# Kernel optimization log

Measured on AMD Instinct MI355X. Metric: run time of the kernel, lower is better.

## Reference

```python
import jax, jax.numpy as jnp
import numpy as np

NUM_GRAPHS = 4096
NODES_PER_GRAPH = 24
EDGES_PER_GRAPH = 48
LG_EDGES_PER_GRAPH = 144
N_ITER = 4
HID = 128
IN_DIM = 70
EDGE_DIM = 6


def seg_softmax(v, seg, num_seg):
    # numerically-stable softmax over segments; v: [E,1]
    m = jax.ops.segment_max(v, seg, num_segments=num_seg)
    e = jnp.exp(v - m[seg])
    s = jax.ops.segment_sum(e, seg, num_segments=num_seg)
    return e / s[seg]


def setup_inputs() -> dict:
    key = jax.random.key(0)
    ks = jax.random.split(key, 20)
    B, NPG, EPG, LPG = NUM_GRAPHS, NODES_PER_GRAPH, EDGES_PER_GRAPH, LG_EDGES_PER_GRAPH
    N, E, LE = B * NPG, B * EPG, B * LPG
    # graph-consistent random connectivity
    goff_n = (jnp.arange(B, dtype=jnp.int32) * NPG)[:, None]
    src = (goff_n + jax.random.randint(ks[0], (B, EPG), 0, NPG)).reshape(-1)
    dst = (goff_n + jax.random.randint(ks[1], (B, EPG), 0, NPG)).reshape(-1)
    edge_index = jnp.stack([src, dst]).astype(jnp.int32)
    goff_e = (jnp.arange(B, dtype=jnp.int32) * EPG)[:, None]
    lsrc = (goff_e + jax.random.randint(ks[2], (B, LPG), 0, EPG)).reshape(-1)
    ldst = (goff_e + jax.random.randint(ks[3], (B, LPG), 0, EPG)).reshape(-1)
    lg_edge_index = jnp.stack([lsrc, ldst]).astype(jnp.int32)
    edge_batch = jnp.repeat(jnp.arange(B, dtype=jnp.int32), EPG)
    s = 0.1
    inp = {
        "x": jax.random.normal(ks[4], (N, IN_DIM), jnp.float32),
        "edge_attr": jax.random.normal(ks[5], (E, EDGE_DIM), jnp.float32),
        "edge_index": edge_index,
        "lg_edge_index": lg_edge_index,
        "edge_batch": edge_batch,
        # params (stored [in, out] so we apply x @ W + b)
        "w_mlp": jax.random.normal(ks[6], (IN_DIM, HID), jnp.float32) * s,
        "b_mlp": jnp.zeros((HID,), jnp.float32),
        "w_u": jax.random.normal(ks[7], (HID, HID), jnp.float32) * s,
        "w_v": jax.random.normal(ks[8], (HID, HID), jnp.float32) * s,
        "w_edge": jax.random.normal(ks[9], (EDGE_DIM, HID), jnp.float32) * s,
        "w_rel": jax.random.normal(ks[10], (HID, 1), jnp.float32) * s,
        "b_rel": jnp.zeros((1,), jnp.float32),
        "w_root": jax.random.normal(ks[11], (HID, 1), jnp.float32) * s,
        "a": jax.random.normal(ks[12], (1, HID, N_ITER), jnp.float32) * s,
        "a_bias": jnp.zeros((1, 1, N_ITER), jnp.float32),
        "w_gout": jax.random.normal(ks[13], (HID, HID), jnp.float32) * s,
        "b_gout": jnp.zeros((HID,), jnp.float32),
        "w_block": jax.random.normal(ks[14], (HID, HID), jnp.float32) * s,
        "b_block": jnp.zeros((HID,), jnp.float32),
    }
    return inp


def reference(x, edge_attr, edge_index, lg_edge_index, edge_batch,
              w_mlp, b_mlp, w_u, w_v, w_edge, w_rel, b_rel, w_root,
              a, a_bias, w_gout, b_gout, w_block, b_block):
    N = x.shape[0]
    src, dst = edge_index[0], edge_index[1]
    lsrc, ldst = lg_edge_index[0], lg_edge_index[1]
    E = src.shape[0]

    # DrugEncoder.mlp
    h = x @ w_mlp + b_mlp  # [N, H]

    # initial directed-edge features: (lin_u(x)[src] + lin_v(x)[dst] + lin_edge(e)) / 3
    e0 = (h @ w_u)[src] + (h @ w_v)[dst] + edge_attr @ w_edge
    e0 = e0 / 3.0  # [E, H]

    out = e0
    outs, gouts = [], []
    for _ in range(N_ITER):
        # line-graph message passing: scatter-add over line-graph edges
        out = e0 + jax.ops.segment_sum(out[lsrc], ldst, num_segments=E)
        # GlobalAttentionPool: GraphConv(H->1) on the line graph, segment softmax, weighted add-pool
        aggr = jax.ops.segment_sum(out[lsrc], ldst, num_segments=E)
        xc = aggr @ w_rel + b_rel + out @ w_root  # [E, 1]
        sc = seg_softmax(xc, edge_batch, NUM_GRAPHS)  # [E, 1]
        g = jax.ops.segment_sum(out * sc, edge_batch, num_segments=NUM_GRAPHS)  # [B, H]
        outs.append(out)
        gouts.append(jnp.tanh(g @ w_gout + b_gout))

    out_all = jnp.stack(outs, axis=-1)    # [E, H, T]
    gout_all = jnp.stack(gouts, axis=-1)  # [B, H, T]

    # temporal attention over iterations
    scores = jnp.einsum('bht,ht->bt', gout_all, a[0])[:, None, :] + a_bias  # [B,1,T]
    scores = jax.nn.softmax(scores, axis=-1)
    per_edge = scores[edge_batch]  # gather == repeat_interleave by per-graph edge counts
    out = (out_all * per_edge).sum(-1)  # [E, H]

    # scatter edge features back to destination nodes
    xo = h + jax.ops.segment_sum(out, dst, num_segments=N)
    xo = xo @ w_block + b_block  # LinearBlock.lin1
    return xo
```

## Files before the change

### kernel.cpp

```cpp
#include <hip/hip_runtime.h>

#define NGR 4096
#define NPG 24
#define EPG 48
#define LPG 144
#define NITER 4
#define HID 128
#define NN (NGR*NPG)
#define NE (NGR*EPG)
#define NL (NGR*LPG)

typedef unsigned int uint;
typedef unsigned short ushort;
typedef short bf16x8 __attribute__((ext_vector_type(8)));
typedef float f32x4 __attribute__((ext_vector_type(4)));
typedef float f32x2 __attribute__((ext_vector_type(2)));

__device__ __forceinline__ float b2f(ushort u){ return __uint_as_float(((uint)u)<<16); }
__device__ __forceinline__ ushort f2b(float f){
  uint x = __float_as_uint(f);
  x += 0x7FFFu + ((x>>16)&1u);
  return (ushort)(x>>16);
}
__device__ __forceinline__ float wredsum(float v){
  #pragma unroll
  for(int m=32;m;m>>=1) v += __shfl_xor(v, m, 64);
  return v;
}
__device__ __forceinline__ f32x4 mfma16(bf16x8 a, bf16x8 b, f32x4 c){
  return __builtin_amdgcn_mfma_f32_16x16x32_bf16(a, b, c, 0, 0, 0);
}

__global__ __launch_bounds__(256) void k_prep(
    const float* __restrict__ wmlp, const float* __restrict__ wu,
    const float* __restrict__ wv, const float* __restrict__ wb,
    ushort* __restrict__ P)
{
  int id = blockIdx.x*256 + threadIdx.x;
  if(id < 12288){
    int n=id/96, k=id-n*96;
    float v=(k<70)? wmlp[k*128+n] : 0.f;
    ushort hb=f2b(v); P[id]=hb; P[12288+id]=f2b(v-b2f(hb));
  } else if(id < 28672){
    int i=id-12288, n=i>>7, k=i&127;
    float v=wu[k*128+n]; ushort hb=f2b(v);
    P[24576+i]=hb; P[40960+i]=f2b(v-b2f(hb));
  } else if(id < 45056){
    int i=id-28672, n=i>>7, k=i&127;
    float v=wv[k*128+n]; ushort hb=f2b(v);
    P[57344+i]=hb; P[73728+i]=f2b(v-b2f(hb));
  } else if(id < 61440){
    int i=id-45056, n=i>>7, k=i&127;
    float v=wb[k*128+n]; ushort hb=f2b(v);
    P[90112+i]=hb; P[106496+i]=f2b(v-b2f(hb));
  }
}

__global__ __launch_bounds__(256,3) void k_fused(
  const float* __restrict__ x, const float* __restrict__ ea,
  const int* __restrict__ eidx, const int* __restrict__ lidx,
  const ushort* __restrict__ P,
  const float* __restrict__ bmlp, const float* __restrict__ wedge,
  const float* __restrict__ wrel, const float* __restrict__ brel,
  const float* __restrict__ wroot,
  const float* __restrict__ aatt, const float* __restrict__ abias,
  const float* __restrict__ wgout, const float* __restrict__ bgout,
  const float* __restrict__ bblock,
  float* __restrict__ out)
{
  const int g=blockIdx.x, tid=threadIdx.x, lane=tid&63, wid=tid>>6;
  const int q=lane>>4, ln=lane&15;
  const int E0=g*EPG, L0=g*LPG;
  const int nA = wid*32 + ln;

  __shared__ __align__(16) char LB[39072];
  ushort* Hh   = (ushort*)(LB + 0);
  ushort* Hl   = (ushort*)(LB + 6528);
  ushort* A_bf = (ushort*)(LB + 13056);
  ushort* A_cnt= (ushort*)(LB + 19968);
  ushort* xh   = (ushort*)(LB + 19968);
  ushort* xl   = (ushort*)(LB + 26112);
  float*  nacc = (float*) (LB + 19968);
  int*    esrc = (int*)   (LB + 32256);
  int*    edst = (int*)   (LB + 32448);
  float*  eaL  = (float*) (LB + 32640);
  float*  Pe   = (float*) (LB + 33792);
  float*  Re   = (float*) (LB + 33984);
  float*  xcs  = (float*) (LB + 34176);
  float*  gsf  = (float*) (LB + 34944);
  float*  sfull= (float*) (LB + 36992);
  float*  score= (float*) (LB + 39040);
  float*  wts  = (float*) (LB + 39056);

  const ushort *WmH=P, *WmL=P+12288, *WuH=P+24576, *WuL=P+40960,
               *WvH=P+57344, *WvL=P+73728, *WbH=P+90112, *WbL=P+106496;
  const f32x4 z4 = {0.f,0.f,0.f,0.f};

  f32x2 gxa[4];
  const f32x2* xg2 = (const f32x2*)(x + (size_t)g*NPG*70);
  #pragma unroll
  for(int i=0;i<4;i++){ int idx=tid+256*i; if(idx<840) gxa[i]=xg2[idx]; }
  for(int idx=tid; idx<1536; idx+=256) ((uint*)A_cnt)[idx]=0u;
  if(tid<48){
    int s=eidx[E0+tid]-g*NPG, d=eidx[NE+E0+tid]-g*NPG;
    esrc[tid]=s; edst[tid]=d; Pe[tid]=0.f; Re[tid]=0.f;
  }
  for(int idx=tid; idx<288; idx+=256) eaL[idx]=ea[(size_t)E0*6+idx];
  for(int idx=tid; idx<512; idx+=256) sfull[idx]=0.f;
  __syncthreads();
  if(tid<LPG){ int ls=lidx[L0+tid]-E0, ld=lidx[NL+L0+tid]-E0;
    atomicAdd(((uint*)A_cnt) + ((ld*64+ls)>>1), 1u<<((ls&1)*16)); }
  __syncthreads();
  for(int idx=tid; idx<48*64; idx+=256){ int i=idx>>6,j=idx&63;
    A_bf[i*72+j]=f2b((float)A_cnt[idx]); }
  __syncthreads();
  #pragma unroll
  for(int i=0;i<4;i++){ int idx=tid+256*i; if(idx<840){
    int r=idx/35, c0=2*(idx-r*35);
    float v0=gxa[i].x, v1=gxa[i].y;
    ushort h0=f2b(v0), h1=f2b(v1);
    xh[r*96+c0]=h0;   xl[r*96+c0]=f2b(v0-b2f(h0));
    xh[r*96+c0+1]=h1; xl[r*96+c0+1]=f2b(v1-b2f(h1)); } }
  for(int idx=tid; idx<624; idx+=256){ int r=idx/26, c=70+(idx-r*26);
    xh[r*96+c]=0; xl[r*96+c]=0; }
  __syncthreads();

  {
    f32x4 hc[2][2];
    #pragma unroll
    for(int mt=0;mt<2;mt++){ hc[mt][0]=z4; hc[mt][1]=z4; }
    #pragma unroll
    for(int kt=0; kt<3; kt++){
      int ko=kt*32+q*8;
      bf16x8 ah0=*(const bf16x8*)&xh[ln*96+ko];
      bf16x8 ah1=*(const bf16x8*)&xh[(16+ln)*96+ko];
      bf16x8 al0=*(const bf16x8*)&xl[ln*96+ko];
      bf16x8 al1=*(const bf16x8*)&xl[(16+ln)*96+ko];
      #pragma unroll
      for(int nt=0;nt<2;nt++){
        int nb=(nA+nt*16)*96+ko;
        bf16x8 bh=*(const bf16x8*)&WmH[nb];
        bf16x8 bl=*(const bf16x8*)&WmL[nb];
        hc[0][nt]=mfma16(ah0,bh,hc[0][nt]);
        hc[0][nt]=mfma16(al0,bh,hc[0][nt]);
        hc[0][nt]=mfma16(ah0,bl,hc[0][nt]);
        hc[1][nt]=mfma16(ah1,bh,hc[1][nt]);
        hc[1][nt]=mfma16(al1,bh,hc[1][nt]);
        hc[1][nt]=mfma16(ah1,bl,hc[1][nt]);
      }
    }
    float bm0=bmlp[nA], bm1=bmlp[nA+16];
    #pragma unroll
    for(int nt=0;nt<2;nt++){ float bb=nt?bm1:bm0; int col=nA+nt*16;
      #pragma unroll
      for(int mt=0;mt<2;mt++)
        #pragma unroll
        for(int r=0;r<4;r++){
          int row=mt*16+q*4+r;
          if(row<24){
            float hvv=hc[mt][nt][r]+bb;
            ushort hb=f2b(hvv);
            Hh[row*136+col]=hb; Hl[row*136+col]=f2b(hvv-b2f(hb));
          }
        }
    }
  }
  __syncthreads();

  f32x4 e0f[3][2];
  {
    int sgm[3], dgm[3];
    #pragma unroll
    for(int mt=0;mt<3;mt++){ sgm[mt]=esrc[mt*16+ln]; dgm[mt]=edst[mt*16+ln]; }
    #pragma unroll
    for(int mt=0;mt<3;mt++){ e0f[mt][0]=z4; e0f[mt][1]=z4; }
    #pragma unroll
    for(int kt=0;kt<4;kt++){
      int ko=kt*32+q*8;
      bf16x8 BuH[2],BuL[2],BvH[2],BvL[2];
      #pragma unroll
      for(int nt=0;nt<2;nt++){
        int nb=(nA+nt*16)*128+ko;
        BuH[nt]=*(const bf16x8*)&WuH[nb]; BuL[nt]=*(const bf16x8*)&WuL[nb];
        BvH[nt]=*(const bf16x8*)&WvH[nb]; BvL[nt]=*(const bf16x8*)&WvL[nb];
      }
      #pragma unroll
      for(int mt=0;mt<3;mt++){
        bf16x8 ash=*(const bf16x8*)&Hh[sgm[mt]*136+ko];
        bf16x8 asl=*(const bf16x8*)&Hl[sgm[mt]*136+ko];
        bf16x8 adh=*(const bf16x8*)&Hh[dgm[mt]*136+ko];
        bf16x8 adl=*(const bf16x8*)&Hl[dgm[mt]*136+ko];
        #pragma unroll
        for(int nt=0;nt<2;nt++){
          f32x4 acc=e0f[mt][nt];
          acc=mfma16(ash,BuH[nt],acc);
          acc=mfma16(asl,BuH[nt],acc);
          acc=mfma16(ash,BuL[nt],acc);
          acc=mfma16(adh,BvH[nt],acc);
          acc=mfma16(adl,BvH[nt],acc);
          acc=mfma16(adh,BvL[nt],acc);
          e0f[mt][nt]=acc;
        }
      }
    }
  }
  {
    const float wrel0=wrel[nA], wrel1=wrel[nA+16];
    const float wroot0=wroot[nA], wroot1=wroot[nA+16];
    float wed0[6],wed1[6];
    #pragma unroll
    for(int k=0;k<6;k++){ wed0[k]=wedge[k*128+nA]; wed1[k]=wedge[k*128+nA+16]; }
    #pragma unroll
    for(int mt=0;mt<3;mt++)
      #pragma unroll
      for(int r=0;r<4;r++){
        int m=mt*16+q*4+r;
        float v0=e0f[mt][0][r], v1=e0f[mt][1][r];
        #pragma unroll
        for(int k=0;k<6;k++){ float e=eaL[m*6+k]; v0+=e*wed0[k]; v1+=e*wed1[k]; }
        e0f[mt][0][r]=v0*(1.f/3.f);
        e0f[mt][1][r]=v1*(1.f/3.f);
      }
    #pragma unroll
    for(int mt=0;mt<3;mt++)
      #pragma unroll
      for(int r=0;r<4;r++){
        float pp=e0f[mt][0][r]*wrel0  + e0f[mt][1][r]*wrel1;
        float rr=e0f[mt][0][r]*wroot0 + e0f[mt][1][r]*wroot1;
        #pragma unroll
        for(int msk=1;msk<16;msk<<=1){ pp+=__shfl_xor(pp,msk,64); rr+=__shfl_xor(rr,msk,64); }
        if(ln==0){ atomicAdd(&Pe[mt*16+q*4+r],pp); atomicAdd(&Re[mt*16+q*4+r],rr); }
      }
  }
  for(int idx=tid; idx<3072; idx+=256) nacc[idx]=0.f;
  __syncthreads();

  if(wid==0){
    const float brel_f=brel[0];
    const int arow=(lane<48)?lane:0;
    float pprev=(lane<48)?Pe[lane]:0.f;
    float rprev=(lane<48)?Re[lane]:0.f;
    const float pe_l=pprev, re_l=rprev;
    float rlast=rprev;
    #pragma unroll
    for(int t=1;t<=5;t++){
      float s=0.f, sr=0.f;
      for(int j=0;j<48;j++){
        float a=b2f(A_bf[arow*72+j]);
        float pj=__shfl(pprev,j,64);
        float rj=__shfl(rprev,j,64);
        s+=a*pj; sr+=a*rj;
      }
      s+=pe_l; sr+=re_l;
      if(t>=2){
        float xv = s - pe_l + rlast + brel_f;
        float v=(lane<48)?xv:-3.0e38f;
        float mx=v;
        #pragma unroll
        for(int msk=32;msk;msk>>=1) mx=fmaxf(mx,__shfl_xor(mx,msk,64));
        float e2=(lane<48)?__expf(v-mx):0.f;
        float ss=e2;
        #pragma unroll
        for(int msk=32;msk;msk>>=1) ss+=__shfl_xor(ss,msk,64);
        if(lane<48) xcs[(t-2)*48+lane]=e2/ss;
      }
      pprev=s; rprev=sr; rlast=sr;
    }
  }
  __syncthreads();

  const int s0=((q&1)<<5)+ln, s1=s0+16;
  const int aoff = ln*72 + q*8;
  {
    f32x4 Ocur[3][2];
    #pragma unroll
    for(int mt=0;mt<3;mt++){ Ocur[mt][0]=e0f[mt][0]; Ocur[mt][1]=e0f[mt][1]; }
    #pragma unroll 1
    for(int t=0;t<NITER;t++){
      #pragma unroll
      for(int nt=0;nt<2;nt++){
        bf16x8 Bh0,Bh1,Bl0,Bl1;
        #pragma unroll
        for(int r=0;r<4;r++){
          float vA0=__shfl(Ocur[0][nt][r],s0), vA1=__shfl(Ocur[1][nt][r],s0);
          float vB0=__shfl(Ocur[0][nt][r],s1), vB1=__shfl(Ocur[1][nt][r],s1);
          float lo_=(q<2)?vA0:vA1, hi_=(q<2)?vB0:vB1;
          ushort u0=f2b(lo_); Bh0[r]=(short)u0;   Bl0[r]=(short)f2b(lo_-b2f(u0));
          ushort u1=f2b(hi_); Bh0[4+r]=(short)u1; Bl0[4+r]=(short)f2b(hi_-b2f(u1));
          float v2a=__shfl(Ocur[2][nt][r],s0), v2b=__shfl(Ocur[2][nt][r],s1);
          float lo2=(q<2)?v2a:0.f, hi2=(q<2)?v2b:0.f;
          ushort u2=f2b(lo2); Bh1[r]=(short)u2;   Bl1[r]=(short)f2b(lo2-b2f(u2));
          ushort u3=f2b(hi2); Bh1[4+r]=(short)u3; Bl1[4+r]=(short)f2b(hi2-b2f(u3));
        }
        #pragma unroll
        for(int mt=0;mt<3;mt++){
          bf16x8 a0=*(const bf16x8*)&A_bf[mt*1152+aoff];
          bf16x8 a1=*(const bf16x8*)&A_bf[mt*1152+aoff+32];
          f32x4 acc=e0f[mt][nt];
          acc=mfma16(a0,Bh0,acc);
          acc=mfma16(a1,Bh1,acc);
          acc=mfma16(a0,Bl0,acc);
          acc=mfma16(a1,Bl1,acc);
          Ocur[mt][nt]=acc;
        }
      }
      float gp0=0.f, gp1=0.f;
      #pragma unroll
      for(int mt=0;mt<3;mt++)
        #pragma unroll
        for(int r=0;r<4;r++){
          float xcv=xcs[t*48+mt*16+q*4+r];
          gp0+=xcv*Ocur[mt][0][r];
          gp1+=xcv*Ocur[mt][1][r];
        }
      gp0+=__shfl_xor(gp0,16,64); gp0+=__shfl_xor(gp0,32,64);
      gp1+=__shfl_xor(gp1,16,64); gp1+=__shfl_xor(gp1,32,64);
      if(q==0){ gsf[t*128+nA]=gp0; gsf[t*128+nA+16]=gp1; }
    }
  }
  __syncthreads();

  {
    float p00=0,p01=0,p10=0,p11=0,p20=0,p21=0,p30=0,p31=0;
    int k0=wid*32;
    for(int kk=0;kk<32;kk++){
      int k=k0+kk;
      f32x2 w=((const f32x2*)wgout)[k*64+lane];
      float g0=gsf[k], g1=gsf[128+k], g2=gsf[256+k], g3=gsf[384+k];
      p00+=g0*w.x; p01+=g0*w.y;
      p10+=g1*w.x; p11+=g1*w.y;
      p20+=g2*w.x; p21+=g2*w.y;
      p30+=g3*w.x; p31+=g3*w.y;
    }
    atomicAdd(&sfull[2*lane],p00);     atomicAdd(&sfull[2*lane+1],p01);
    atomicAdd(&sfull[128+2*lane],p10); atomicAdd(&sfull[128+2*lane+1],p11);
    atomicAdd(&sfull[256+2*lane],p20); atomicAdd(&sfull[256+2*lane+1],p21);
    atomicAdd(&sfull[384+2*lane],p30); atomicAdd(&sfull[384+2*lane+1],p31);
  }
  __syncthreads();
  {
    int t=wid;
    float s0v=sfull[t*128+2*lane]  +bgout[2*lane];
    float s1v=sfull[t*128+2*lane+1]+bgout[2*lane+1];
    float v=tanhf(s0v)*aatt[(2*lane)*4+t]+tanhf(s1v)*aatt[(2*lane+1)*4+t];
    v=wredsum(v);
    if(lane==0) score[t]=v+abias[t];
  }
  __syncthreads();
  if(tid==0){
    float m=fmaxf(fmaxf(score[0],score[1]),fmaxf(score[2],score[3]));
    float e0v=__expf(score[0]-m), e1v=__expf(score[1]-m),
          e2v=__expf(score[2]-m), e3v=__expf(score[3]-m);
    float s=e0v+e1v+e2v+e3v;
    wts[0]=e0v/s; wts[1]=e1v/s; wts[2]=e2v/s; wts[3]=e3v/s;
  }
  __syncthreads();

  {
    const float cc4=wts[3], cc3=cc4+wts[2], cc2=cc3+wts[1];
    f32x4 Z[3][2];
    #pragma unroll
    for(int mt=0;mt<3;mt++)
      #pragma unroll
      for(int nt=0;nt<2;nt++)
        #pragma unroll
        for(int r=0;r<4;r++) Z[mt][nt][r]=cc4*e0f[mt][nt][r];
    #pragma unroll 1
    for(int s=0;s<NITER;s++){
      const float ci = (s==0)?cc3:(s==1)?cc2:1.f;
      #pragma unroll
      for(int nt=0;nt<2;nt++){
        bf16x8 Bh0,Bh1,Bl0,Bl1;
        #pragma unroll
        for(int r=0;r<4;r++){
          float vA0=__shfl(Z[0][nt][r],s0), vA1=__shfl(Z[1][nt][r],s0);
          float vB0=__shfl(Z[0][nt][r],s1), vB1=__shfl(Z[1][nt][r],s1);
          float lo_=(q<2)?vA0:vA1, hi_=(q<2)?vB0:vB1;
          ushort u0=f2b(lo_); Bh0[r]=(short)u0;   Bl0[r]=(short)f2b(lo_-b2f(u0));
          ushort u1=f2b(hi_); Bh0[4+r]=(short)u1; Bl0[4+r]=(short)f2b(hi_-b2f(u1));
          float v2a=__shfl(Z[2][nt][r],s0), v2b=__shfl(Z[2][nt][r],s1);
          float lo2=(q<2)?v2a:0.f, hi2=(q<2)?v2b:0.f;
          ushort u2=f2b(lo2); Bh1[r]=(short)u2;   Bl1[r]=(short)f2b(lo2-b2f(u2));
          ushort u3=f2b(hi2); Bh1[4+r]=(short)u3; Bl1[4+r]=(short)f2b(hi2-b2f(u3));
        }
        #pragma unroll
        for(int mt=0;mt<3;mt++){
          bf16x8 a0=*(const bf16x8*)&A_bf[mt*1152+aoff];
          bf16x8 a1=*(const bf16x8*)&A_bf[mt*1152+aoff+32];
          f32x4 acc;
          #pragma unroll
          for(int r=0;r<4;r++) acc[r]=ci*e0f[mt][nt][r];
          acc=mfma16(a0,Bh0,acc);
          acc=mfma16(a1,Bh1,acc);
          acc=mfma16(a0,Bl0,acc);
          acc=mfma16(a1,Bl1,acc);
          Z[mt][nt]=acc;
        }
      }
    }
    #pragma unroll
    for(int mt=0;mt<3;mt++)
      #pragma unroll
      for(int nt=0;nt<2;nt++){
        int ncol=nA+nt*16;
        #pragma unroll
        for(int r=0;r<4;r++){
          int dn=edst[mt*16+q*4+r];
          atomicAdd(&nacc[dn*128+ncol],Z[mt][nt][r]);
        }
      }
  }
  __syncthreads();
  for(int idx=tid; idx<24*128; idx+=256){
    int n=idx>>7, k=idx&127;
    float zv=b2f(Hh[n*136+k])+b2f(Hl[n*136+k])+nacc[idx];
    ushort hb=f2b(zv);
    Hh[n*136+k]=hb; Hl[n*136+k]=f2b(zv-b2f(hb));
  }
  __syncthreads();
  {
    f32x4 c4[2][2];
    c4[0][0]=z4; c4[0][1]=z4; c4[1][0]=z4; c4[1][1]=z4;
    #pragma unroll
    for(int kt=0;kt<4;kt++){
      int ko=kt*32+q*8;
      bf16x8 ah0=*(const bf16x8*)&Hh[ln*136+ko];
      bf16x8 ah1=*(const bf16x8*)&Hh[(16+ln)*136+ko];
      bf16x8 al0=*(const bf16x8*)&Hl[ln*136+ko];
      bf16x8 al1=*(const bf16x8*)&Hl[(16+ln)*136+ko];
      #pragma unroll
      for(int nt=0;nt<2;nt++){
        int nb=(nA+nt*16)*128+ko;
        bf16x8 bh=*(const bf16x8*)&WbH[nb];
        bf16x8 bl=*(const bf16x8*)&WbL[nb];
        c4[0][nt]=mfma16(ah0,bh,c4[0][nt]);
        c4[0][nt]=mfma16(al0,bh,c4[0][nt]);
        c4[0][nt]=mfma16(ah0,bl,c4[0][nt]);
        c4[1][nt]=mfma16(ah1,bh,c4[1][nt]);
        c4[1][nt]=mfma16(al1,bh,c4[1][nt]);
        c4[1][nt]=mfma16(ah1,bl,c4[1][nt]);
      }
    }
    float bb0=bblock[nA], bb1=bblock[nA+16];
    #pragma unroll
    for(int nt=0;nt<2;nt++){ float bbx=nt?bb1:bb0; int col=nA+nt*16;
      #pragma unroll
      for(int mt=0;mt<2;mt++)
        #pragma unroll
        for(int r=0;r<4;r++){
          int row=mt*16+q*4+r;
          if(row<24) out[(size_t)(g*NPG+row)*128+col]=c4[mt][nt][r]+bbx;
        }
    }
  }
}

extern "C" void kernel_launch(void* const* d_in, const int* in_sizes, int n_in,
                              void* d_out, int out_size, void* d_ws, size_t ws_size,
                              hipStream_t stream)
{
  (void)in_sizes; (void)n_in; (void)out_size; (void)ws_size;
  const float* x      = (const float*)d_in[0];
  const float* eattr  = (const float*)d_in[1];
  const int*   eidx   = (const int*)d_in[2];
  const int*   lidx   = (const int*)d_in[3];
  const float* wmlp   = (const float*)d_in[5];
  const float* bmlp   = (const float*)d_in[6];
  const float* wu     = (const float*)d_in[7];
  const float* wvv    = (const float*)d_in[8];
  const float* wedge  = (const float*)d_in[9];
  const float* wrel   = (const float*)d_in[10];
  const float* brel   = (const float*)d_in[11];
  const float* wroot  = (const float*)d_in[12];
  const float* aatt   = (const float*)d_in[13];
  const float* abias  = (const float*)d_in[14];
  const float* wgout  = (const float*)d_in[15];
  const float* bgout  = (const float*)d_in[16];
  const float* wblock = (const float*)d_in[17];
  const float* bblock = (const float*)d_in[18];

  ushort* P = (ushort*)d_ws;

  k_prep <<<240, 256, 0, stream>>>(wmlp, wu, wvv, wblock, P);
  k_fused<<<NGR, 256, 0, stream>>>(x, eattr, eidx, lidx, P,
                                   bmlp, wedge, wrel, brel, wroot,
                                   aatt, abias, wgout, bgout, bblock,
                                   (float*)d_out);
}
```

Before: 571.3 us.

## Stage line-graph propagation operand through LDS instead of cross-lane shuffles

The B operand for the line-graph MFMA propagation was rebuilt from accumulator registers with many __shfl calls per iteration. It is now written to a per-column float buffer in LDS and read back as vectorized f32x4 loads before splitting into hi/lo bf16. The adjacency matrix stride shrinks from 72 to 56, and the unused K padding is served by a small zero buffer, which moves the nacc zeroing later and adds barriers. LDS use grows from about 39KB to 50KB per block, which may limit occupancy under the launch bound of 3 blocks.

```diff
diff --git a/kernel.cpp b/kernel.cpp
--- a/kernel.cpp
+++ b/kernel.cpp
@@ -73,24 +73,26 @@
   const int E0=g*EPG, L0=g*LPG;
   const int nA = wid*32 + ln;
 
-  __shared__ __align__(16) char LB[39072];
+  __shared__ __align__(16) char LB[50368];
   ushort* Hh   = (ushort*)(LB + 0);
   ushort* Hl   = (ushort*)(LB + 6528);
   ushort* A_bf = (ushort*)(LB + 13056);
-  ushort* A_cnt= (ushort*)(LB + 19968);
-  ushort* xh   = (ushort*)(LB + 19968);
-  ushort* xl   = (ushort*)(LB + 26112);
-  float*  nacc = (float*) (LB + 19968);
-  int*    esrc = (int*)   (LB + 32256);
-  int*    edst = (int*)   (LB + 32448);
-  float*  eaL  = (float*) (LB + 32640);
-  float*  Pe   = (float*) (LB + 33792);
-  float*  Re   = (float*) (LB + 33984);
-  float*  xcs  = (float*) (LB + 34176);
-  float*  gsf  = (float*) (LB + 34944);
-  float*  sfull= (float*) (LB + 36992);
-  float*  score= (float*) (LB + 39040);
-  float*  wts  = (float*) (LB + 39056);
+  ushort* A_cnt= (ushort*)(LB + 18432);
+  ushort* xh   = (ushort*)(LB + 18432);
+  ushort* xl   = (ushort*)(LB + 24576);
+  float*  Pe   = (float*) (LB + 30720);
+  float*  Re   = (float*) (LB + 30912);
+  float*  eaL  = (float*) (LB + 31104);
+  float*  OUTf = (float*) (LB + 18432);
+  float*  nacc = (float*) (LB + 18432);
+  int*    esrc = (int*)   (LB + 45056);
+  int*    edst = (int*)   (LB + 45248);
+  float*  xcs  = (float*) (LB + 45440);
+  float*  gsf  = (float*) (LB + 46208);
+  float*  sfull= (float*) (LB + 48256);
+  float*  score= (float*) (LB + 50304);
+  float*  wts  = (float*) (LB + 50320);
+  float*  zeroF= (float*) (LB + 50336);
 
   const ushort *WmH=P, *WmL=P+12288, *WuH=P+24576, *WuL=P+40960,
                *WvH=P+57344, *WvL=P+73728, *WbH=P+90112, *WbL=P+106496;
@@ -105,14 +107,15 @@
     int s=eidx[E0+tid]-g*NPG, d=eidx[NE+E0+tid]-g*NPG;
     esrc[tid]=s; edst[tid]=d; Pe[tid]=0.f; Re[tid]=0.f;
   }
+  if(tid<8) zeroF[tid]=0.f;
   for(int idx=tid; idx<288; idx+=256) eaL[idx]=ea[(size_t)E0*6+idx];
   for(int idx=tid; idx<512; idx+=256) sfull[idx]=0.f;
   __syncthreads();
   if(tid<LPG){ int ls=lidx[L0+tid]-E0, ld=lidx[NL+L0+tid]-E0;
     atomicAdd(((uint*)A_cnt) + ((ld*64+ls)>>1), 1u<<((ls&1)*16)); }
   __syncthreads();
-  for(int idx=tid; idx<48*64; idx+=256){ int i=idx>>6,j=idx&63;
-    A_bf[i*72+j]=f2b((float)A_cnt[idx]); }
+  for(int idx=tid; idx<48*48; idx+=256){ int i=idx/48, j=idx-i*48;
+    A_bf[i*56+j]=f2b((float)A_cnt[i*64+j]); }
   __syncthreads();
   #pragma unroll
   for(int i=0;i<4;i++){ int idx=tid+256*i; if(idx<840){
@@ -232,7 +235,6 @@
         if(ln==0){ atomicAdd(&Pe[mt*16+q*4+r],pp); atomicAdd(&Re[mt*16+q*4+r],rr); }
       }
   }
-  for(int idx=tid; idx<3072; idx+=256) nacc[idx]=0.f;
   __syncthreads();
 
   if(wid==0){
@@ -246,7 +248,7 @@
     for(int t=1;t<=5;t++){
       float s=0.f, sr=0.f;
       for(int j=0;j<48;j++){
-        float a=b2f(A_bf[arow*72+j]);
+        float a=b2f(A_bf[arow*56+j]);
         float pj=__shfl(pprev,j,64);
         float rj=__shfl(rprev,j,64);
         s+=a*pj; sr+=a*rj;
@@ -269,54 +271,60 @@
   }
   __syncthreads();
 
-  const int s0=((q&1)<<5)+ln, s1=s0+16;
-  const int aoff = ln*72 + q*8;
-  {
-    f32x4 Ocur[3][2];
-    #pragma unroll
-    for(int mt=0;mt<3;mt++){ Ocur[mt][0]=e0f[mt][0]; Ocur[mt][1]=e0f[mt][1]; }
-    #pragma unroll 1
-    for(int t=0;t<NITER;t++){
-      #pragma unroll
-      for(int nt=0;nt<2;nt++){
-        bf16x8 Bh0,Bh1,Bl0,Bl1;
-        #pragma unroll
-        for(int r=0;r<4;r++){
-          float vA0=__shfl(Ocur[0][nt][r],s0), vA1=__shfl(Ocur[1][nt][r],s0);
-          float vB0=__shfl(Ocur[0][nt][r],s1), vB1=__shfl(Ocur[1][nt][r],s1);
-          float lo_=(q<2)?vA0:vA1, hi_=(q<2)?vB0:vB1;
-          ushort u0=f2b(lo_); Bh0[r]=(short)u0;   Bl0[r]=(short)f2b(lo_-b2f(u0));
-          ushort u1=f2b(hi_); Bh0[4+r]=(short)u1; Bl0[4+r]=(short)f2b(hi_-b2f(u1));
-          float v2a=__shfl(Ocur[2][nt][r],s0), v2b=__shfl(Ocur[2][nt][r],s1);
-          float lo2=(q<2)?v2a:0.f, hi2=(q<2)?v2b:0.f;
-          ushort u2=f2b(lo2); Bh1[r]=(short)u2;   Bl1[r]=(short)f2b(lo2-b2f(u2));
-          ushort u3=f2b(hi2); Bh1[4+r]=(short)u3; Bl1[4+r]=(short)f2b(hi2-b2f(u3));
-        }
-        #pragma unroll
-        for(int mt=0;mt<3;mt++){
-          bf16x8 a0=*(const bf16x8*)&A_bf[mt*1152+aoff];
-          bf16x8 a1=*(const bf16x8*)&A_bf[mt*1152+aoff+32];
-          f32x4 acc=e0f[mt][nt];
-          acc=mfma16(a0,Bh0,acc);
-          acc=mfma16(a1,Bh1,acc);
-          acc=mfma16(a0,Bl0,acc);
-          acc=mfma16(a1,Bl1,acc);
-          Ocur[mt][nt]=acc;
-        }
-      }
-      float gp0=0.f, gp1=0.f;
+  f32x4 Ocur[3][2];
+  #pragma unroll
+  for(int mt=0;mt<3;mt++)
+    #pragma unroll
+    for(int nt=0;nt<2;nt++)
+      *(f32x4*)&OUTf[(nA+nt*16)*52 + mt*16 + q*4] = e0f[mt][nt];
+  #pragma unroll 1
+  for(int t=0;t<NITER;t++){
+    #pragma unroll
+    for(int nt=0;nt<2;nt++){
+      const float* Bcol = &OUTf[(nA+nt*16)*52];
+      f32x4 b0a=*(const f32x4*)&Bcol[q*8];
+      f32x4 b0b=*(const f32x4*)&Bcol[q*8+4];
+      const float* pb1 = (q<2)? &Bcol[32+q*8] : zeroF;
+      f32x4 b1a=*(const f32x4*)pb1;
+      f32x4 b1b=*(const f32x4*)(pb1+4);
+      bf16x8 Bh0,Bl0,Bh1,Bl1;
+      #pragma unroll
+      for(int j=0;j<4;j++){
+        ushort h;
+        h=f2b(b0a[j]); Bh0[j]=(short)h;   Bl0[j]=(short)f2b(b0a[j]-b2f(h));
+        h=f2b(b0b[j]); Bh0[4+j]=(short)h; Bl0[4+j]=(short)f2b(b0b[j]-b2f(h));
+        h=f2b(b1a[j]); Bh1[j]=(short)h;   Bl1[j]=(short)f2b(b1a[j]-b2f(h));
+        h=f2b(b1b[j]); Bh1[4+j]=(short)h; Bl1[4+j]=(short)f2b(b1b[j]-b2f(h));
+      }
+      #pragma unroll
+      for(int mt=0;mt<3;mt++){
+        int ar=(mt*16+ln)*56;
+        bf16x8 a0=*(const bf16x8*)&A_bf[ar+q*8];
+        const ushort* pa1=(q<2)? &A_bf[ar+32+q*8] : (const ushort*)zeroF;
+        bf16x8 a1=*(const bf16x8*)pa1;
+        f32x4 acc=e0f[mt][nt];
+        acc=mfma16(a0,Bh0,acc);
+        acc=mfma16(a1,Bh1,acc);
+        acc=mfma16(a0,Bl0,acc);
+        acc=mfma16(a1,Bl1,acc);
+        Ocur[mt][nt]=acc;
+      }
       #pragma unroll
       for(int mt=0;mt<3;mt++)
-        #pragma unroll
-        for(int r=0;r<4;r++){
-          float xcv=xcs[t*48+mt*16+q*4+r];
-          gp0+=xcv*Ocur[mt][0][r];
-          gp1+=xcv*Ocur[mt][1][r];
-        }
-      gp0+=__shfl_xor(gp0,16,64); gp0+=__shfl_xor(gp0,32,64);
-      gp1+=__shfl_xor(gp1,16,64); gp1+=__shfl_xor(gp1,32,64);
-      if(q==0){ gsf[t*128+nA]=gp0; gsf[t*128+nA+16]=gp1; }
-    }
+        *(f32x4*)&OUTf[(nA+nt*16)*52 + mt*16 + q*4] = Ocur[mt][nt];
+    }
+    float gp0=0.f, gp1=0.f;
+    #pragma unroll
+    for(int mt=0;mt<3;mt++)
+      #pragma unroll
+      for(int r=0;r<4;r++){
+        float xcv=xcs[t*48+mt*16+q*4+r];
+        gp0+=xcv*Ocur[mt][0][r];
+        gp1+=xcv*Ocur[mt][1][r];
+      }
+    gp0+=__shfl_xor(gp0,16,64); gp0+=__shfl_xor(gp0,32,64);
+    gp1+=__shfl_xor(gp1,16,64); gp1+=__shfl_xor(gp1,32,64);
+    if(q==0){ gsf[t*128+nA]=gp0; gsf[t*128+nA+16]=gp1; }
   }
   __syncthreads();
 
@@ -362,31 +370,37 @@
     #pragma unroll
     for(int mt=0;mt<3;mt++)
       #pragma unroll
-      for(int nt=0;nt<2;nt++)
+      for(int nt=0;nt<2;nt++){
         #pragma unroll
         for(int r=0;r<4;r++) Z[mt][nt][r]=cc4*e0f[mt][nt][r];
+        *(f32x4*)&OUTf[(nA+nt*16)*52 + mt*16 + q*4] = Z[mt][nt];
+      }
     #pragma unroll 1
     for(int s=0;s<NITER;s++){
       const float ci = (s==0)?cc3:(s==1)?cc2:1.f;
       #pragma unroll
       for(int nt=0;nt<2;nt++){
-        bf16x8 Bh0,Bh1,Bl0,Bl1;
-        #pragma unroll
-        for(int r=0;r<4;r++){
-          float vA0=__shfl(Z[0][nt][r],s0), vA1=__shfl(Z[1][nt][r],s0);
-          float vB0=__shfl(Z[0][nt][r],s1), vB1=__shfl(Z[1][nt][r],s1);
-          float lo_=(q<2)?vA0:vA1, hi_=(q<2)?vB0:vB1;
-          ushort u0=f2b(lo_); Bh0[r]=(short)u0;   Bl0[r]=(short)f2b(lo_-b2f(u0));
-          ushort u1=f2b(hi_); Bh0[4+r]=(short)u1; Bl0[4+r]=(short)f2b(hi_-b2f(u1));
-          float v2a=__shfl(Z[2][nt][r],s0), v2b=__shfl(Z[2][nt][r],s1);
-          float lo2=(q<2)?v2a:0.f, hi2=(q<2)?v2b:0.f;
-          ushort u2=f2b(lo2); Bh1[r]=(short)u2;   Bl1[r]=(short)f2b(lo2-b2f(u2));
-          ushort u3=f2b(hi2); Bh1[4+r]=(short)u3; Bl1[4+r]=(short)f2b(hi2-b2f(u3));
+        const float* Bcol = &OUTf[(nA+nt*16)*52];
+        f32x4 b0a=*(const f32x4*)&Bcol[q*8];
+        f32x4 b0b=*(const f32x4*)&Bcol[q*8+4];
+        const float* pb1 = (q<2)? &Bcol[32+q*8] : zeroF;
+        f32x4 b1a=*(const f32x4*)pb1;
+        f32x4 b1b=*(const f32x4*)(pb1+4);
+        bf16x8 Bh0,Bl0,Bh1,Bl1;
+        #pragma unroll
+        for(int j=0;j<4;j++){
+          ushort h;
+          h=f2b(b0a[j]); Bh0[j]=(short)h;   Bl0[j]=(short)f2b(b0a[j]-b2f(h));
+          h=f2b(b0b[j]); Bh0[4+j]=(short)h; Bl0[4+j]=(short)f2b(b0b[j]-b2f(h));
+          h=f2b(b1a[j]); Bh1[j]=(short)h;   Bl1[j]=(short)f2b(b1a[j]-b2f(h));
+          h=f2b(b1b[j]); Bh1[4+j]=(short)h; Bl1[4+j]=(short)f2b(b1b[j]-b2f(h));
         }
         #pragma unroll
         for(int mt=0;mt<3;mt++){
-          bf16x8 a0=*(const bf16x8*)&A_bf[mt*1152+aoff];
-          bf16x8 a1=*(const bf16x8*)&A_bf[mt*1152+aoff+32];
+          int ar=(mt*16+ln)*56;
+          bf16x8 a0=*(const bf16x8*)&A_bf[ar+q*8];
+          const ushort* pa1=(q<2)? &A_bf[ar+32+q*8] : (const ushort*)zeroF;
+          bf16x8 a1=*(const bf16x8*)pa1;
           f32x4 acc;
           #pragma unroll
           for(int r=0;r<4;r++) acc[r]=ci*e0f[mt][nt][r];
@@ -396,8 +410,16 @@
           acc=mfma16(a1,Bl1,acc);
           Z[mt][nt]=acc;
         }
-      }
-    }
+        if(s<NITER-1){
+          #pragma unroll
+          for(int mt=0;mt<3;mt++)
+            *(f32x4*)&OUTf[(nA+nt*16)*52 + mt*16 + q*4] = Z[mt][nt];
+        }
+      }
+    }
+    __syncthreads();
+    for(int idx=tid; idx<3072; idx+=256) nacc[idx]=0.f;
+    __syncthreads();
     #pragma unroll
     for(int mt=0;mt<3;mt++)
       #pragma unroll
```

After: 547.9 us. -4.1%, faster.
